# Performance work log

Hardware: AMD Instinct MI355X
Metric: run time of the kernel (lower is better)

Reference implementation:

```python
import jax, jax.numpy as jnp
import numpy as np
from jax import lax

# retina / model config (matches init_kwargs)
G, K, S = 64, 3, 2            # first patch size, n scales, scale factor
B, C, H, W = 64, 3, 512, 512  # input batch
C1, C2 = 64, 128              # feature extractor channels


def setup_inputs() -> dict:
    key = jax.random.key(0)
    k1, k2, k3, k4 = jax.random.split(key, 4)
    x = jax.random.normal(k1, (B, C, H, W), jnp.float32)
    # normalized fixation coords in [-1, 1]
    l = jax.random.uniform(k2, (B, 2), jnp.float32, minval=-1.0, maxval=1.0)
    w1 = jax.random.normal(k3, (C1, C, 3, 3), jnp.float32) * 0.05
    b1 = jnp.zeros((C1,), jnp.float32)
    w2 = jax.random.normal(k4, (C2, C1, 3, 3), jnp.float32) * 0.05
    b2 = jnp.zeros((C2,), jnp.float32)
    return {"x": x, "l": l, "w1": w1, "b1": b1, "w2": w2, "b2": b2}


def _conv(x, w, stride):
    return lax.conv_general_dilated(
        x, w, (stride, stride), 'SAME',
        dimension_numbers=('NCHW', 'OIHW', 'NCHW'))


def _extract_patches(x, coords, size):
    """Batched equivalent of crude_retina.extract_patch.

    Torch pads by size//2+1 only when the crop exceeds the image; padding
    unconditionally and offsetting the start indices yields identical values.
    x: (B,C,H,W), coords: (B,2) int [y,x]. Returns (B,C,size,size).
    """
    pad = size // 2 + 1
    xp = jnp.pad(x, ((0, 0), (0, 0), (pad, pad), (pad, pad)))
    start_y = coords[:, 0] - size // 2 + pad
    start_x = coords[:, 1] - size // 2 + pad

    def slice_one(im, sy, sx):
        return lax.dynamic_slice(im, (0, sy, sx), (im.shape[0], size, size))

    return jax.vmap(slice_one)(xp, start_y, start_x)


def _resize_nearest(p, g):
    # torch F.interpolate(mode='nearest'): src = floor(dst * in/out)
    size = p.shape[-1]
    idx = (jnp.arange(g) * size) // g
    return p[:, :, idx][:, :, :, idx]


def reference(x, l, w1, b1, w2, b2):
    T = jnp.array([H, W], jnp.float32)
    # to_exocentric: floor(0.5*(l+1)*T) clamped to [0, max(H,W)]
    coords = jnp.clip(jnp.floor(0.5 * (l + 1.0) * T), 0, max(H, W)).astype(jnp.int32)

    # multi-scale foveation
    phi = []
    size = G
    for _ in range(K):
        p = _extract_patches(x, coords, size)
        if size != G:
            p = _resize_nearest(p, G)
        phi.append(p)
        size = int(S * size)
    phi = jnp.stack(phi, axis=1)  # (B, K, C, G, G)

    # feature extractor applied per patch scale
    outs = []
    for i in range(K):
        h = jax.nn.relu(_conv(phi[:, i], w1, 1) + b1[:, None, None])
        h = jax.nn.relu(_conv(h, w2, 2) + b2[:, None, None])
        outs.append(h)
    return jnp.stack(outs, axis=1)  # (B, K, C2, G//2, G//2)
```

## Files before the change

### kernel.cpp

```cpp
#include <hip/hip_runtime.h>
#include <hip/hip_bf16.h>

typedef __attribute__((ext_vector_type(4))) float  f32x4;
typedef __attribute__((ext_vector_type(8))) _Float16 f16x8;

static __device__ __forceinline__ void gld_lds16(const void* g, void* l) {
    __builtin_amdgcn_global_load_lds(
        (const __attribute__((address_space(1))) void*)g,
        (__attribute__((address_space(3))) void*)l, 16, 0, 0);
}

__global__ void transform_kernel(const float* __restrict__ w1, const float* __restrict__ w2,
                                 _Float16* __restrict__ Bt1, _Float16* __restrict__ Bt2)
{
    const int i = blockIdx.x * 256 + threadIdx.x;
    if (i < 64 * 32) {
        const int n = i >> 5, k = i & 31;
        const float v = (k < 27) ? w1[n * 27 + k] : 0.0f;
        Bt1[i] = (_Float16)v;
    }
    const int j = i - 64 * 32;
    if (j >= 0 && j < 9 * 128 * 64) {
        const int tap = j / (128 * 64);
        const int rem = j % (128 * 64);
        const int n = rem >> 6;
        const int c1 = rem & 63;
        Bt2[j] = (_Float16)w2[((size_t)n * 64 + c1) * 9 + tap];
    }
}

__global__ __launch_bounds__(256) void conv1_mfma(
    const float* __restrict__ x, const float* __restrict__ l,
    const _Float16* __restrict__ Bt1, const float* __restrict__ b1,
    _Float16* __restrict__ h1, int bk0)
{
    const int img = blockIdx.y;
    const int bk  = bk0 + img;
    const int b   = bk / 3, ksc = bk % 3;
    const int step = 1 << ksc;
    const int half = 32 << ksc;
    const int py0 = blockIdx.x * 4;

    const float ly = l[b * 2 + 0], lx = l[b * 2 + 1];
    int cy = (int)floorf(0.5f * (ly + 1.0f) * 512.0f);
    int cx = (int)floorf(0.5f * (lx + 1.0f) * 512.0f);
    cy = min(max(cy, 0), 512);
    cx = min(max(cx, 0), 512);
    const int sy = cy - half, sx = cx - half;

    __shared__ float    patch[3 * 6 * 66];
    __shared__ _Float16 out_t[256 * 64];

    const int t = threadIdx.x;
    const float* xb = x + (size_t)b * 3 * 512 * 512;
    for (int i = t; i < 3 * 6 * 66; i += 256) {
        const int c  = i / 396, r = i % 396;
        const int ry = r / 66, xx = r % 66;
        const int yy = py0 - 1 + ry;
        const int col = xx - 1;
        const int iy = sy + yy * step, ix = sx + col * step;
        float v = 0.0f;
        if (yy >= 0 && yy < 64 && col >= 0 && col < 64 &&
            iy >= 0 && iy < 512 && ix >= 0 && ix < 512)
            v = xb[(size_t)c * 262144 + iy * 512 + ix];
        patch[i] = v;
    }
    __syncthreads();

    const int wave = t >> 6, lane = t & 63;
    const int lrow = lane & 15, kb = lane >> 4;

    int offj[8];
    #pragma unroll
    for (int j = 0; j < 8; ++j) {
        const int k  = kb * 8 + j;
        const int c  = (k * 57) >> 9;
        const int rr = k - c * 9;
        const int kh = (rr * 43) >> 7;
        const int kw = rr - kh * 3;
        offj[j] = (k < 27) ? (c * 396 + kh * 66 + kw) : -1;
    }

    f16x8 bfr[4];
    #pragma unroll
    for (int nf = 0; nf < 4; ++nf)
        bfr[nf] = *(const f16x8*)(Bt1 + ((size_t)(nf * 16 + lrow)) * 32 + kb * 8);

    f32x4 acc[4][4];
    #pragma unroll
    for (int mf = 0; mf < 4; ++mf)
        #pragma unroll
        for (int nf = 0; nf < 4; ++nf)
            #pragma unroll
            for (int r = 0; r < 4; ++r) acc[mf][nf][r] = 0.0f;

    #pragma unroll
    for (int mf = 0; mf < 4; ++mf) {
        const int pix  = (wave * 4 + mf) * 16 + lrow;
        const int pbase = (pix >> 6) * 66 + (pix & 63);
        f16x8 afr;
        #pragma unroll
        for (int j = 0; j < 8; ++j)
            afr[j] = (offj[j] >= 0) ? (_Float16)patch[offj[j] + pbase] : (_Float16)0.0f;
        #pragma unroll
        for (int nf = 0; nf < 4; ++nf)
            acc[mf][nf] = __builtin_amdgcn_mfma_f32_16x16x32_f16(afr, bfr[nf], acc[mf][nf], 0, 0, 0);
    }

    #pragma unroll
    for (int mf = 0; mf < 4; ++mf) {
        const int ml0 = (wave * 4 + mf) * 16 + kb * 4;
        #pragma unroll
        for (int nf = 0; nf < 4; ++nf) {
            const int c1 = nf * 16 + lrow;
            const float bb = b1[c1];
            #pragma unroll
            for (int r = 0; r < 4; ++r) {
                const float v = fmaxf(acc[mf][nf][r] + bb, 0.0f);
                const int ml = ml0 + r;
                const int xcol = ml & 63;
                const int psx = ((xcol & 1) << 5) | (xcol >> 1);
                const int pl  = (ml & ~63) | psx;
                const int c1s = c1 ^ ((psx & 7) << 3);
                out_t[pl * 64 + c1s] = (_Float16)v;
            }
        }
    }
    __syncthreads();

    _Float16* hb = h1 + (size_t)img * 4096 * 64 + (size_t)py0 * 64 * 64;
    #pragma unroll
    for (int j = 0; j < 8; ++j) {
        const int idx = j * 256 + t;
        *(f16x8*)(hb + (size_t)idx * 8) = *(const f16x8*)&out_t[idx * 8];
    }
}

__global__ __launch_bounds__(256) void conv2_mfma(
    const _Float16* __restrict__ h1, const _Float16* __restrict__ Bt2,
    const float* __restrict__ b2, float* __restrict__ out, int bk0)
{
    const int img = blockIdx.y;
    const int bk  = bk0 + img;
    const int mc  = blockIdx.x;
    const int t = threadIdx.x, wave = t >> 6, lane = t & 63;
    const int lrow = lane & 15, kb = lane >> 4;
    const int wq = wave >> 1;
    const int wn = wave & 1;

    __shared__ _Float16 As[5 * 4096 + 2 * 8192];
    _Float16* Bs = As + 5 * 4096;

    const _Float16* hb = h1 + (size_t)img * 4096 * 64;
    const int ys = mc * 4;
    const int nrows = (mc == 15) ? 4 : 5;

    if (mc == 15) {
        f16x8 z = {};
        *(f16x8*)&As[4 * 4096 + t * 16]     = z;
        *(f16x8*)&As[4 * 4096 + t * 16 + 8] = z;
    }

    {
        const _Float16* ga = hb + (size_t)ys * 4096;
        #pragma unroll
        for (int j = 0; j < 10; ++j) {
            if (j < nrows * 2) {
                const int c = j * 256 + t;
                gld_lds16(ga + (size_t)c * 8, As + (j * 256 + wave * 64) * 8);
            }
        }
    }
    {
        #pragma unroll
        for (int i = 0; i < 4; ++i) {
            const int c = i * 256 + t;
            const int r = c >> 3, j = c & 7;
            const int jt = j ^ (r & 7);
            gld_lds16(Bt2 + (size_t)r * 64 + jt * 8,
                      Bs + (i * 256 + wave * 64) * 8);
        }
    }

    f32x4 acc[2][4];
    #pragma unroll
    for (int mf = 0; mf < 2; ++mf)
        #pragma unroll
        for (int nf = 0; nf < 4; ++nf)
            #pragma unroll
            for (int r = 0; r < 4; ++r) acc[mf][nf][r] = 0.0f;

    #pragma unroll 1
    for (int tap = 0; tap < 9; ++tap) {
        __syncthreads();
        if (tap < 8) {
            const _Float16* gb = Bt2 + (size_t)(tap + 1) * 8192;
            const int slot = (tap + 1) & 1;
            #pragma unroll
            for (int i = 0; i < 4; ++i) {
                const int c = i * 256 + t;
                const int r = c >> 3, j = c & 7;
                const int jt = j ^ (r & 7);
                gld_lds16(gb + (size_t)r * 64 + jt * 8,
                          Bs + slot * 8192 + (i * 256 + wave * 64) * 8);
            }
        }
        const int kh = tap / 3, kw = tap % 3;
        const int par = kw & 1;
        const int rrow = 2 * wq + kh;
        const int slot = tap & 1;

        #pragma unroll
        for (int c1h = 0; c1h < 2; ++c1h) {
            const int jt = c1h * 4 + kb;
            f16x8 afr[2];
            #pragma unroll
            for (int mf = 0; mf < 2; ++mf) {
                const int ox = mf * 16 + lrow;
                const int xh = ox + (kw >> 1);
                const int p  = rrow * 64 + par * 32 + xh;
                f16x8 v = *(const f16x8*)&As[p * 64 + (jt ^ (p & 7)) * 8];
                if ((kw == 2) && (ox == 31)) v = (f16x8){};
                afr[mf] = v;
            }
            #pragma unroll
            for (int nf = 0; nf < 4; ++nf) {
                const int r = wn * 64 + nf * 16 + lrow;
                const f16x8 bfr = *(const f16x8*)&Bs[slot * 8192 + r * 64 + (jt ^ (r & 7)) * 8];
                #pragma unroll
                for (int mf = 0; mf < 2; ++mf)
                    acc[mf][nf] = __builtin_amdgcn_mfma_f32_16x16x32_f16(afr[mf], bfr, acc[mf][nf], 0, 0, 0);
            }
        }
    }

    float* ob = out + (size_t)bk * 128 * 1024;
    #pragma unroll
    for (int mf = 0; mf < 2; ++mf) {
        const int m0 = mc * 64 + wq * 32 + mf * 16 + kb * 4;
        #pragma unroll
        for (int nf = 0; nf < 4; ++nf) {
            const int c2 = wn * 64 + nf * 16 + lrow;
            const float bb = b2[c2];
            f32x4 v;
            #pragma unroll
            for (int r = 0; r < 4; ++r) v[r] = fmaxf(acc[mf][nf][r] + bb, 0.0f);
            *(f32x4*)(ob + (size_t)c2 * 1024 + m0) = v;
        }
    }
}

extern "C" void kernel_launch(void* const* d_in, const int* in_sizes, int n_in,
                              void* d_out, int out_size, void* d_ws, size_t ws_size,
                              hipStream_t stream) {
    const float* x  = (const float*)d_in[0];
    const float* l  = (const float*)d_in[1];
    const float* w1 = (const float*)d_in[2];
    const float* b1 = (const float*)d_in[3];
    const float* w2 = (const float*)d_in[4];
    const float* b2 = (const float*)d_in[5];
    float* out = (float*)d_out;

    _Float16* Bt1 = (_Float16*)d_ws;
    _Float16* Bt2 = Bt1 + 64 * 32;
    _Float16* h1  = (_Float16*)((char*)d_ws + 160 * 1024);

    const int total_imgs = 192;
    const size_t per_img = (size_t)4096 * 64 * sizeof(_Float16);
    size_t h1_cap = (ws_size > 160 * 1024) ? ws_size - 160 * 1024 : 0;
    int ipc = (int)(h1_cap / per_img);
    if (ipc > total_imgs) ipc = total_imgs;
    if (ipc < 1) ipc = 1;

    transform_kernel<<<296, 256, 0, stream>>>(w1, w2, Bt1, Bt2);

    for (int bk0 = 0; bk0 < total_imgs; bk0 += ipc) {
        const int n = (total_imgs - bk0 < ipc) ? (total_imgs - bk0) : ipc;
        conv1_mfma<<<dim3(16, n), 256, 0, stream>>>(x, l, Bt1, b1, h1, bk0);
        conv2_mfma<<<dim3(16, n), 256, 0, stream>>>(h1, Bt2, b2, out, bk0);
    }
}
```

Baseline: 100.3 us.

## Pipeline conv2 weight loads in half-tap stages with 4-slot ring buffer

Splits each conv2 weight tap into two 32-channel halves and streams them through a four-slot LDS ring, keeping three stages in flight. Explicit vmcnt waits and raw s_barrier replace the per-tap __syncthreads, so weight fetches overlap the MFMA work instead of being drained each tap. The B tile swizzle changes to match the narrower 32-element rows. The trade is more barriers per tap and hand-managed waitcnts whose counts must match the async load pattern exactly.

```diff
diff --git a/kernel.cpp b/kernel.cpp
--- a/kernel.cpp
+++ b/kernel.cpp
@@ -96,7 +96,7 @@
 
     #pragma unroll
     for (int mf = 0; mf < 4; ++mf) {
-        const int pix  = (wave * 4 + mf) * 16 + lrow;
+        const int pix   = (wave * 4 + mf) * 16 + lrow;
         const int pbase = (pix >> 6) * 66 + (pix & 63);
         f16x8 afr;
         #pragma unroll
@@ -148,7 +148,7 @@
     const int wq = wave >> 1;
     const int wn = wave & 1;
 
-    __shared__ _Float16 As[5 * 4096 + 2 * 8192];
+    __shared__ _Float16 As[5 * 4096 + 4 * 4096];
     _Float16* Bs = As + 5 * 4096;
 
     const _Float16* hb = h1 + (size_t)img * 4096 * 64;
@@ -171,16 +171,23 @@
             }
         }
     }
-    {
-        #pragma unroll
-        for (int i = 0; i < 4; ++i) {
-            const int c = i * 256 + t;
-            const int r = c >> 3, j = c & 7;
-            const int jt = j ^ (r & 7);
-            gld_lds16(Bt2 + (size_t)r * 64 + jt * 8,
-                      Bs + (i * 256 + wave * 64) * 8);
-        }
-    }
+
+#define BSTAGE(u)                                                                 \
+    {                                                                             \
+        const int tap_ = (u) >> 1, c1h_ = (u) & 1, slot_ = (u) & 3;               \
+        _Pragma("unroll")                                                         \
+        for (int i = 0; i < 2; ++i) {                                             \
+            const int c  = i * 256 + t;                                           \
+            const int r  = c >> 2, jh = c & 3;                                    \
+            const int js = jh ^ ((r >> 1) & 3);                                   \
+            gld_lds16(Bt2 + (size_t)tap_ * 8192 + r * 64 + c1h_ * 32 + js * 8,    \
+                      Bs + slot_ * 4096 + (i * 256 + wave * 64) * 8);             \
+        }                                                                         \
+    }
+
+    BSTAGE(0)
+    BSTAGE(1)
+    BSTAGE(2)
 
     f32x4 acc[2][4];
     #pragma unroll
@@ -191,46 +198,39 @@
             for (int r = 0; r < 4; ++r) acc[mf][nf][r] = 0.0f;
 
     #pragma unroll 1
-    for (int tap = 0; tap < 9; ++tap) {
-        __syncthreads();
-        if (tap < 8) {
-            const _Float16* gb = Bt2 + (size_t)(tap + 1) * 8192;
-            const int slot = (tap + 1) & 1;
-            #pragma unroll
-            for (int i = 0; i < 4; ++i) {
-                const int c = i * 256 + t;
-                const int r = c >> 3, j = c & 7;
-                const int jt = j ^ (r & 7);
-                gld_lds16(gb + (size_t)r * 64 + jt * 8,
-                          Bs + slot * 8192 + (i * 256 + wave * 64) * 8);
-            }
-        }
+    for (int u = 0; u < 18; ++u) {
+        if (u <= 15)      asm volatile("s_waitcnt vmcnt(4)" ::: "memory");
+        else if (u == 16) asm volatile("s_waitcnt vmcnt(2)" ::: "memory");
+        else              asm volatile("s_waitcnt vmcnt(0)" ::: "memory");
+        __builtin_amdgcn_s_barrier();
+        __builtin_amdgcn_sched_barrier(0);
+
+        if (u + 3 < 18) BSTAGE(u + 3)
+
+        const int tap = u >> 1, c1h = u & 1;
         const int kh = tap / 3, kw = tap % 3;
         const int par = kw & 1;
         const int rrow = 2 * wq + kh;
-        const int slot = tap & 1;
-
-        #pragma unroll
-        for (int c1h = 0; c1h < 2; ++c1h) {
-            const int jt = c1h * 4 + kb;
-            f16x8 afr[2];
-            #pragma unroll
-            for (int mf = 0; mf < 2; ++mf) {
-                const int ox = mf * 16 + lrow;
-                const int xh = ox + (kw >> 1);
-                const int p  = rrow * 64 + par * 32 + xh;
-                f16x8 v = *(const f16x8*)&As[p * 64 + (jt ^ (p & 7)) * 8];
-                if ((kw == 2) && (ox == 31)) v = (f16x8){};
-                afr[mf] = v;
-            }
-            #pragma unroll
-            for (int nf = 0; nf < 4; ++nf) {
-                const int r = wn * 64 + nf * 16 + lrow;
-                const f16x8 bfr = *(const f16x8*)&Bs[slot * 8192 + r * 64 + (jt ^ (r & 7)) * 8];
-                #pragma unroll
-                for (int mf = 0; mf < 2; ++mf)
-                    acc[mf][nf] = __builtin_amdgcn_mfma_f32_16x16x32_f16(afr[mf], bfr, acc[mf][nf], 0, 0, 0);
-            }
+        const int jt = c1h * 4 + kb;
+        const int slot = u & 3;
+
+        f16x8 afr[2];
+        #pragma unroll
+        for (int mf = 0; mf < 2; ++mf) {
+            const int ox = mf * 16 + lrow;
+            const int xh = ox + (kw >> 1);
+            const int p  = rrow * 64 + par * 32 + xh;
+            f16x8 v = *(const f16x8*)&As[p * 64 + (jt ^ (p & 7)) * 8];
+            if ((kw == 2) && (ox == 31)) v = (f16x8){};
+            afr[mf] = v;
+        }
+        #pragma unroll
+        for (int nf = 0; nf < 4; ++nf) {
+            const int r = wn * 64 + nf * 16 + lrow;
+            const f16x8 bfr = *(const f16x8*)&Bs[slot * 4096 + r * 32 + (kb ^ ((r >> 1) & 3)) * 8];
+            #pragma unroll
+            for (int mf = 0; mf < 2; ++mf)
+                acc[mf][nf] = __builtin_amdgcn_mfma_f32_16x16x32_f16(afr[mf], bfr, acc[mf][nf], 0, 0, 0);
         }
     }
 
```

Measured after the change: 106.5 us. 1.06x slower.
